# Kernel optimization log

Hardware: AMD Instinct MI355X
Metric: run time of the kernel (lower is better)

## Reference

```python
import jax, jax.numpy as jnp
import numpy as np

MARGIN = jnp.float32(0.0)


def setup_inputs() -> dict:
    key = jax.random.key(0)
    k1, k2 = jax.random.split(key)
    cos_pred = jax.random.uniform(k1, (4096, 8192), dtype=jnp.float32)
    mask_gt = jax.random.randint(k2, (4096, 8192), 0, 2, dtype=jnp.int32)
    return {"cos_pred": cos_pred, "mask_gt": mask_gt}


def reference(cos_pred, mask_gt):
    # RankerEmbLoss with rank_type == 'avg', margin == 0.0, fully vectorized:
    # per row i: mean over gt entries of (1 - cos), mean over non-gt entries of
    # relu(cos - margin); then average means over rows.
    mask = mask_gt.astype(bool)                      # [n_docs, n_qs]
    n_qs = cos_pred.shape[1]
    cnt_t = jnp.sum(mask, axis=1).astype(cos_pred.dtype)          # positives per row
    cnt_nt = (n_qs - cnt_t).astype(cos_pred.dtype)                # negatives per row
    sum_t = jnp.sum(jnp.where(mask, 1.0 - cos_pred, 0.0), axis=1)
    sum_nt = jnp.sum(jnp.where(mask, 0.0, jnp.maximum(cos_pred - MARGIN, 0.0)), axis=1)
    loss_tgt = jnp.mean(sum_t / cnt_t)
    loss_nontgt = jnp.mean(sum_nt / cnt_nt)
    loss = (loss_tgt + loss_nontgt) * 0.5
    return (loss, loss_tgt, loss_nontgt)
```

## Files before the change

### kernel.cpp

```cpp
#include <hip/hip_runtime.h>

constexpr int N_DOCS = 4096;
constexpr int N_QS   = 8192;
constexpr int BLOCK  = 256;
constexpr int VEC_PER_THREAD = N_QS / 4 / BLOCK;

typedef float fx4 __attribute__((ext_vector_type(4)));
typedef int   ix4 __attribute__((ext_vector_type(4)));

__global__ __launch_bounds__(BLOCK) void row_reduce_kernel(
    const fx4* __restrict__ cos4,
    const ix4* __restrict__ mask4,
    float2* __restrict__ row_out)
{
    const int row = blockIdx.x;
    const int tid = threadIdx.x;
    const long base = (long)row * (N_QS / 4);

    fx4 c[VEC_PER_THREAD];
    ix4 m[VEC_PER_THREAD];
#pragma unroll
    for (int v = 0; v < VEC_PER_THREAD; ++v) {
        const int idx = v * BLOCK + tid;
        c[v] = __builtin_nontemporal_load(&cos4[base + idx]);
        m[v] = __builtin_nontemporal_load(&mask4[base + idx]);
    }
    __builtin_amdgcn_sched_barrier(0);

    float s_mc = 0.f, s_nt = 0.f;
    int   icnt = 0;
#pragma unroll
    for (int v = 0; v < VEC_PER_THREAD; ++v) {
        s_mc += (m[v].x != 0) ? c[v].x : 0.f;
        s_mc += (m[v].y != 0) ? c[v].y : 0.f;
        s_mc += (m[v].z != 0) ? c[v].z : 0.f;
        s_mc += (m[v].w != 0) ? c[v].w : 0.f;

        s_nt += (m[v].x != 0) ? 0.f : fmaxf(c[v].x, 0.f);
        s_nt += (m[v].y != 0) ? 0.f : fmaxf(c[v].y, 0.f);
        s_nt += (m[v].z != 0) ? 0.f : fmaxf(c[v].z, 0.f);
        s_nt += (m[v].w != 0) ? 0.f : fmaxf(c[v].w, 0.f);

        icnt += m[v].x + m[v].y + m[v].z + m[v].w;
    }

    float cf = (float)icnt;
#pragma unroll
    for (int off = 32; off > 0; off >>= 1) {
        s_mc += __shfl_down(s_mc, off);
        s_nt += __shfl_down(s_nt, off);
        cf   += __shfl_down(cf,   off);
    }

    __shared__ float red_mc[4], red_nt[4], red_c[4];
    const int wave = tid >> 6;
    const int lane = tid & 63;
    if (lane == 0) {
        red_mc[wave] = s_mc;
        red_nt[wave] = s_nt;
        red_c[wave]  = cf;
    }
    __syncthreads();

    if (tid == 0) {
        float mc = 0.f, nt = 0.f, ct = 0.f;
#pragma unroll
        for (int w = 0; w < 4; ++w) { mc += red_mc[w]; nt += red_nt[w]; ct += red_c[w]; }
        float t      = ct - mc;
        float cnt_nt = (float)N_QS - ct;
        row_out[row] = make_float2(t / ct, nt / cnt_nt);
    }
}

__global__ __launch_bounds__(1024) void final_reduce_kernel(
    const float2* __restrict__ row_out,
    float* __restrict__ out)
{
    const int tid = threadIdx.x;
    float a = 0.f, b = 0.f;
#pragma unroll
    for (int i = tid; i < N_DOCS; i += 1024) {
        float2 r = row_out[i];
        a += r.x;
        b += r.y;
    }
#pragma unroll
    for (int off = 32; off > 0; off >>= 1) {
        a += __shfl_down(a, off);
        b += __shfl_down(b, off);
    }
    __shared__ float sa[16], sb[16];
    const int wave = tid >> 6;
    const int lane = tid & 63;
    if (lane == 0) { sa[wave] = a; sb[wave] = b; }
    __syncthreads();
    if (tid == 0) {
        float ta = 0.f, tb = 0.f;
#pragma unroll
        for (int w = 0; w < 16; ++w) { ta += sa[w]; tb += sb[w]; }
        float loss_tgt    = ta / (float)N_DOCS;
        float loss_nontgt = tb / (float)N_DOCS;
        out[0] = (loss_tgt + loss_nontgt) * 0.5f;
        out[1] = loss_tgt;
        out[2] = loss_nontgt;
    }
}

extern "C" void kernel_launch(void* const* d_in, const int* in_sizes, int n_in,
                              void* d_out, int out_size, void* d_ws, size_t ws_size,
                              hipStream_t stream) {
    const fx4* cos4  = (const fx4*)d_in[0];
    const ix4* mask4 = (const ix4*)d_in[1];
    float2* row_out = (float2*)d_ws;
    float*  out     = (float*)d_out;

    row_reduce_kernel<<<N_DOCS, BLOCK, 0, stream>>>(cos4, mask4, row_out);
    final_reduce_kernel<<<1, 1024, 0, stream>>>(row_out, out);
}
```

Measured before the change: 249.2 us.

## Assign one wave per row and stream loads in chunks

Each row is now reduced by a single 64-lane wave instead of a whole 256-thread block, so four rows share a block and the grid shrinks by four. The LDS reduction and __syncthreads are removed. Loads are issued in chunks of eight vectors inside an unrolled loop, replacing the single bulk load of all data into registers. This aims to cut block-level sync overhead and register pressure while keeping enough loads in flight to saturate memory bandwidth. The risk is less memory-level parallelism per wave if the compiler serializes the chunks.

```diff
diff --git a/kernel.cpp b/kernel.cpp
--- a/kernel.cpp
+++ b/kernel.cpp
@@ -3,7 +3,12 @@
 constexpr int N_DOCS = 4096;
 constexpr int N_QS   = 8192;
 constexpr int BLOCK  = 256;
-constexpr int VEC_PER_THREAD = N_QS / 4 / BLOCK;
+constexpr int WAVES_PER_BLOCK = BLOCK / 64;
+constexpr int GRID  = N_DOCS / WAVES_PER_BLOCK;
+constexpr int VECS_PER_ROW = N_QS / 4;
+constexpr int VECS_PER_LANE = VECS_PER_ROW / 64;
+constexpr int CHUNK = 8;
+constexpr int N_CHUNKS = VECS_PER_LANE / CHUNK;
 
 typedef float fx4 __attribute__((ext_vector_type(4)));
 typedef int   ix4 __attribute__((ext_vector_type(4)));
@@ -13,35 +18,38 @@
     const ix4* __restrict__ mask4,
     float2* __restrict__ row_out)
 {
-    const int row = blockIdx.x;
-    const int tid = threadIdx.x;
-    const long base = (long)row * (N_QS / 4);
-
-    fx4 c[VEC_PER_THREAD];
-    ix4 m[VEC_PER_THREAD];
-#pragma unroll
-    for (int v = 0; v < VEC_PER_THREAD; ++v) {
-        const int idx = v * BLOCK + tid;
-        c[v] = __builtin_nontemporal_load(&cos4[base + idx]);
-        m[v] = __builtin_nontemporal_load(&mask4[base + idx]);
-    }
-    __builtin_amdgcn_sched_barrier(0);
+    const int tid  = threadIdx.x;
+    const int lane = tid & 63;
+    const int row  = blockIdx.x * WAVES_PER_BLOCK + (tid >> 6);
+    const long base = (long)row * VECS_PER_ROW + lane;
 
     float s_mc = 0.f, s_nt = 0.f;
     int   icnt = 0;
+
 #pragma unroll
-    for (int v = 0; v < VEC_PER_THREAD; ++v) {
-        s_mc += (m[v].x != 0) ? c[v].x : 0.f;
-        s_mc += (m[v].y != 0) ? c[v].y : 0.f;
-        s_mc += (m[v].z != 0) ? c[v].z : 0.f;
-        s_mc += (m[v].w != 0) ? c[v].w : 0.f;
+    for (int ch = 0; ch < N_CHUNKS; ++ch) {
+        fx4 c[CHUNK];
+        ix4 m[CHUNK];
+#pragma unroll
+        for (int v = 0; v < CHUNK; ++v) {
+            const long idx = base + (long)(ch * CHUNK + v) * 64;
+            c[v] = __builtin_nontemporal_load(&cos4[idx]);
+            m[v] = __builtin_nontemporal_load(&mask4[idx]);
+        }
+#pragma unroll
+        for (int v = 0; v < CHUNK; ++v) {
+            s_mc += (m[v].x != 0) ? c[v].x : 0.f;
+            s_mc += (m[v].y != 0) ? c[v].y : 0.f;
+            s_mc += (m[v].z != 0) ? c[v].z : 0.f;
+            s_mc += (m[v].w != 0) ? c[v].w : 0.f;
 
-        s_nt += (m[v].x != 0) ? 0.f : fmaxf(c[v].x, 0.f);
-        s_nt += (m[v].y != 0) ? 0.f : fmaxf(c[v].y, 0.f);
-        s_nt += (m[v].z != 0) ? 0.f : fmaxf(c[v].z, 0.f);
-        s_nt += (m[v].w != 0) ? 0.f : fmaxf(c[v].w, 0.f);
+            s_nt += (m[v].x != 0) ? 0.f : fmaxf(c[v].x, 0.f);
+            s_nt += (m[v].y != 0) ? 0.f : fmaxf(c[v].y, 0.f);
+            s_nt += (m[v].z != 0) ? 0.f : fmaxf(c[v].z, 0.f);
+            s_nt += (m[v].w != 0) ? 0.f : fmaxf(c[v].w, 0.f);
 
-        icnt += m[v].x + m[v].y + m[v].z + m[v].w;
+            icnt += m[v].x + m[v].y + m[v].z + m[v].w;
+        }
     }
 
     float cf = (float)icnt;
@@ -52,23 +60,10 @@
         cf   += __shfl_down(cf,   off);
     }
 
-    __shared__ float red_mc[4], red_nt[4], red_c[4];
-    const int wave = tid >> 6;
-    const int lane = tid & 63;
     if (lane == 0) {
-        red_mc[wave] = s_mc;
-        red_nt[wave] = s_nt;
-        red_c[wave]  = cf;
-    }
-    __syncthreads();
-
-    if (tid == 0) {
-        float mc = 0.f, nt = 0.f, ct = 0.f;
-#pragma unroll
-        for (int w = 0; w < 4; ++w) { mc += red_mc[w]; nt += red_nt[w]; ct += red_c[w]; }
-        float t      = ct - mc;
-        float cnt_nt = (float)N_QS - ct;
-        row_out[row] = make_float2(t / ct, nt / cnt_nt);
+        float t      = cf - s_mc;
+        float cnt_nt = (float)N_QS - cf;
+        row_out[row] = make_float2(t / cf, s_nt / cnt_nt);
     }
 }
 
@@ -114,6 +109,6 @@
     float2* row_out = (float2*)d_ws;
     float*  out     = (float*)d_out;
 
-    row_reduce_kernel<<<N_DOCS, BLOCK, 0, stream>>>(cos4, mask4, row_out);
+    row_reduce_kernel<<<GRID, BLOCK, 0, stream>>>(cos4, mask4, row_out);
     final_reduce_kernel<<<1, 1024, 0, stream>>>(row_out, out);
 }
```

Result: no change. 249.4 us (+0.1%).
